# Optimization experiments

Measured on AMD Instinct MI355X. Metric: run time of the kernel, lower is better.

The kernel has to match this reference:

```python
import jax, jax.numpy as jnp
import numpy as np

N_NODES = 100000
N_EDGES = 1000000
F_IN = 8
HID = 64
VOCAB = 64
TXT_F = 64
SEQ = 10
N_CLASSES = 2


def setup_inputs() -> dict:
    key = jax.random.key(0)
    ks = jax.random.split(key, 16)
    inp = {
        "x": jax.random.normal(ks[0], (N_NODES, F_IN), dtype=jnp.float32),
        "edge_index": jax.random.randint(ks[1], (2, N_EDGES), 0, N_NODES, dtype=jnp.int32),
        "xtext": jax.random.randint(ks[2], (N_NODES, SEQ), 0, VOCAB, dtype=jnp.int32),
        # GCN layers (PyG convention: out = norm_agg(x @ W) + b)
        "conv1_w": jax.random.normal(ks[3], (F_IN, HID), dtype=jnp.float32) * 0.2,
        "conv1_b": jnp.zeros((HID,), jnp.float32),
        "conv2_w": jax.random.normal(ks[4], (HID, HID), dtype=jnp.float32) * 0.1,
        "conv2_b": jnp.zeros((HID,), jnp.float32),
        # embedding + GRU (torch layout: w_ih [3H, in], w_hh [3H, H])
        "embed": jax.random.normal(ks[5], (VOCAB, TXT_F), dtype=jnp.float32) * 0.1,
        "gru_w_ih": jax.random.normal(ks[6], (3 * HID, TXT_F), dtype=jnp.float32) * 0.1,
        "gru_w_hh": jax.random.normal(ks[7], (3 * HID, HID), dtype=jnp.float32) * 0.1,
        "gru_b_ih": jnp.zeros((3 * HID,), jnp.float32),
        "gru_b_hh": jnp.zeros((3 * HID,), jnp.float32),
        # pair MLPs (torch Linear layout: [out, in])
        "lin1_w": jax.random.normal(ks[8], (HID, 2 * HID), dtype=jnp.float32) * 0.1,
        "lin1_b": jnp.zeros((HID,), jnp.float32),
        "lin_text_w": jax.random.normal(ks[9], (HID, 2 * HID), dtype=jnp.float32) * 0.1,
        "lin_text_b": jnp.zeros((HID,), jnp.float32),
        "lin_final_w": jax.random.normal(ks[10], (N_CLASSES, 2 * HID), dtype=jnp.float32) * 0.1,
        "lin_final_b": jnp.zeros((N_CLASSES,), jnp.float32),
    }
    return inp


def _gcn_norm(edge_index, n_nodes):
    # PyG GCNConv default: add self loops, symmetric normalization
    loops = jnp.arange(n_nodes, dtype=edge_index.dtype)
    src = jnp.concatenate([edge_index[0], loops])
    dst = jnp.concatenate([edge_index[1], loops])
    deg = jax.ops.segment_sum(jnp.ones_like(dst, dtype=jnp.float32), dst, num_segments=n_nodes)
    dinv = jnp.where(deg > 0, jax.lax.rsqrt(deg), 0.0)
    norm = dinv[src] * dinv[dst]  # [E+N]
    return src, dst, norm


def _gcn(h, src, dst, norm, W, b, n_nodes):
    h = h @ W                              # [N, out]
    msg = h[src] * norm[:, None]           # gather + scale
    out = jax.ops.segment_sum(msg, dst, num_segments=n_nodes)
    return out + b


def _gru_last(xe, w_ih, w_hh, b_ih, b_hh):
    # xe: [N, T, F]; returns last hidden state [N, H]
    H = w_hh.shape[1]
    gi_all = jnp.einsum('ntf,gf->ntg', xe, w_ih) + b_ih  # precompute input gates [N,T,3H]
    gi_all = jnp.transpose(gi_all, (1, 0, 2))            # [T, N, 3H]

    def step(h, gi):
        gh = h @ w_hh.T + b_hh
        i_r, i_z, i_n = jnp.split(gi, 3, axis=-1)
        h_r, h_z, h_n = jnp.split(gh, 3, axis=-1)
        r = jax.nn.sigmoid(i_r + h_r)
        z = jax.nn.sigmoid(i_z + h_z)
        n = jnp.tanh(i_n + r * h_n)
        h = (1.0 - z) * n + z * h
        return h, None

    h0 = jnp.zeros((xe.shape[0], H), xe.dtype)
    h_last, _ = jax.lax.scan(step, h0, gi_all)
    return h_last


def reference(x, edge_index, xtext,
              conv1_w, conv1_b, conv2_w, conv2_b,
              embed, gru_w_ih, gru_w_hh, gru_b_ih, gru_b_hh,
              lin1_w, lin1_b, lin_text_w, lin_text_b, lin_final_w, lin_final_b):
    n = x.shape[0]
    src, dst, norm = _gcn_norm(edge_index, n)

    h = jax.nn.relu(_gcn(x, src, dst, norm, conv1_w, conv1_b, n))
    h = jax.nn.relu(_gcn(h, src, dst, norm, conv2_w, conv2_b, n))

    xe = embed[xtext]                                   # [N, T, F]
    textout = _gru_last(xe, gru_w_ih, gru_w_hh, gru_b_ih, gru_b_hh)  # [N, 64]

    s, t = edge_index[0], edge_index[1]
    xpair = jnp.concatenate([h[s], h[t]], axis=1)       # [E, 128]
    xpair = jax.nn.relu(xpair @ lin1_w.T + lin1_b)

    xpairtext = jnp.concatenate([textout[s], textout[t]], axis=1)
    xpairtext = jax.nn.relu(xpairtext @ lin_text_w.T + lin_text_b)

    xfin = jnp.concatenate([xpair, xpairtext], axis=1) @ lin_final_w.T + lin_final_b
    return jax.nn.log_softmax(xfin, axis=1)
```

## Files before the change

kernel.cpp:

```cpp
#include <hip/hip_runtime.h>
#include <stdint.h>

#define N_NODES 100000
#define N_EDGES 1000000
#define NBLK 391

typedef unsigned short u16;
typedef unsigned int u32;
typedef __attribute__((ext_vector_type(8))) short bshort8;
typedef __attribute__((ext_vector_type(4))) float f32x4;

__device__ __forceinline__ float bf2f(u16 u){ union{float f; u32 i;} x; x.i=((u32)u)<<16; return x.f; }
__device__ __forceinline__ u16 f2bf(float f){ union{float f; u32 i;} x; x.f=f; u32 r = x.i + 0x7FFFu + ((x.i>>16)&1u); return (u16)(r>>16); }

__device__ __forceinline__ float fexp2(float x){
#if __has_builtin(__builtin_amdgcn_exp2f)
    return __builtin_amdgcn_exp2f(x);
#else
    return exp2f(x);
#endif
}
__device__ __forceinline__ float frcp(float x){
#if __has_builtin(__builtin_amdgcn_rcpf)
    return __builtin_amdgcn_rcpf(x);
#else
    return 1.0f/x;
#endif
}
#define LOG2E 1.442695041f

__global__ void k_detect(const u16* __restrict__ x, int* flagp){
    __shared__ int cnt;
    if(threadIdx.x == 0) cnt = 0;
    __syncthreads();
    int c = 0;
    for(int i = threadIdx.x; i < 2048; i += 256){
        int e = (x[i] >> 7) & 0xFF;
        if(e >= 0x90) c++;
    }
    atomicAdd(&cnt, c);
    __syncthreads();
    if(threadIdx.x == 0) flagp[0] = (cnt > 64) ? 1 : 0;
}

#define CX    0
#define CW1   800000
#define CB1   800512
#define CW2   800576
#define CB2   804672
#define CEMB  804736
#define CWIH  808832
#define CWHH  821120
#define CBIH  833408
#define CBHH  833600
#define CL1W  833792
#define CL1B  841984
#define CLTW  842048
#define CLTB  850240
#define CLFW  850304
#define CLFB  850560
#define CTOT  850562

__device__ __forceinline__ float ldany(const void* p, int i, int fl){
    return fl ? ((const float*)p)[i] : bf2f(((const u16*)p)[i]);
}

#define NCONV 3323
#define B_W2  (NCONV)
#define B_WHH (B_W2 + 16)
#define B_L1A (B_WHH + 48)
#define B_L1B (B_L1A + 16)
#define B_LTA (B_L1B + 16)
#define B_LTB (B_LTA + 16)
#define B_GIT (B_LTB + 16)
#define B_TOT (B_GIT + 48)

__device__ __forceinline__ void packb_dev(const void* src, u16* dst,
                                          int K, int N, int ldk, int ldn,
                                          int fl, int i){
    if(i >= K*N) return;
    int k = i / N, n = i % N;
    int kt = k >> 5, kk = k & 31, q = kk >> 3, j = kk & 7;
    int nt = n >> 4, nn = n & 15;
    int KT = K >> 5;
    dst[(((nt*KT + kt)*64) + (q*16 + nn))*8 + j] = f2bf(ldany(src, k*ldk + n*ldn, fl));
}

__global__ void k_tables(const int* __restrict__ flagp,
                         const void* x, const void* w1, const void* b1, const void* w2,
                         const void* b2, const void* emb, const void* wih, const void* whh,
                         const void* bih, const void* bhh, const void* l1w, const void* l1b,
                         const void* ltw, const void* ltb, const void* lfw, const void* lfb,
                         float* __restrict__ canon,
                         u16* __restrict__ w2p, u16* __restrict__ whhp,
                         u16* __restrict__ l1pa, u16* __restrict__ l1pb,
                         u16* __restrict__ ltpa, u16* __restrict__ ltpb,
                         float* __restrict__ giT){
    int b = blockIdx.x, tid = threadIdx.x;
    int fl = *flagp;
    if(b < NCONV){
        int i = b*256 + tid;
        if(i >= CTOT) return;
        const void* p; int off;
        if     (i < CW1 ){ p = x;   off = i;        }
        else if(i < CB1 ){ p = w1;  off = i - CW1;  }
        else if(i < CW2 ){ p = b1;  off = i - CB1;  }
        else if(i < CB2 ){ p = w2;  off = i - CW2;  }
        else if(i < CEMB){ p = b2;  off = i - CB2;  }
        else if(i < CWIH){ p = emb; off = i - CEMB; }
        else if(i < CWHH){ p = wih; off = i - CWIH; }
        else if(i < CBIH){ p = whh; off = i - CWHH; }
        else if(i < CBHH){ p = bih; off = i - CBIH; }
        else if(i < CL1W){ p = bhh; off = i - CBHH; }
        else if(i < CL1B){ p = l1w; off = i - CL1W; }
        else if(i < CLTW){ p = l1b; off = i - CL1B; }
        else if(i < CLTB){ p = ltw; off = i - CLTW; }
        else if(i < CLFW){ p = ltb; off = i - CLTB; }
        else if(i < CLFB){ p = lfw; off = i - CLFW; }
        else             { p = lfb; off = i - CLFB; }
        float v = ldany(p, off, fl);
        canon[i] = (v == v && fabsf(v) < 1e30f) ? v : 0.f;
    }else if(b < B_WHH){
        packb_dev(w2, w2p, 64, 64, 64, 1, fl, (b - B_W2)*256 + tid);
    }else if(b < B_L1A){
        packb_dev(whh, whhp, 64, 192, 1, 64, fl, (b - B_WHH)*256 + tid);
    }else if(b < B_L1B){
        packb_dev(l1w, l1pa, 64, 64, 1, 128, fl, (b - B_L1A)*256 + tid);
    }else if(b < B_LTA){
        packb_dev((const void*)((const char*)l1w + (fl ? 64*4 : 64*2)),
                  l1pb, 64, 64, 1, 128, fl, (b - B_L1B)*256 + tid);
    }else if(b < B_LTB){
        packb_dev(ltw, ltpa, 64, 64, 1, 128, fl, (b - B_LTA)*256 + tid);
    }else if(b < B_GIT){
        packb_dev((const void*)((const char*)ltw + (fl ? 64*4 : 64*2)),
                  ltpb, 64, 64, 1, 128, fl, (b - B_LTB)*256 + tid);
    }else{
        int i = (b - B_GIT)*256 + tid;
        if(i >= 64*192) return;
        int v = i / 192, g = i % 192;
        float acc = ldany(bih, g, fl) + ((g < 128) ? ldany(bhh, g, fl) : 0.0f);
        for(int f = 0; f < 64; f++) acc += ldany(wih, g*64 + f, fl) * ldany(emb, v*64 + f, fl);
        int g3 = g >> 6, rem = g & 63, t = rem >> 4, col = rem & 15;
        giT[(((size_t)v*3 + g3)*16 + col)*4 + t] = acc;
    }
}

__global__ void k_hist(const int* __restrict__ ei, int* __restrict__ deg){
    int e = blockIdx.x*256 + threadIdx.x;
    if(e < N_EDGES) atomicAdd(&deg[ei[N_EDGES + e]], 1);
}
__global__ void k_scan1(const int* __restrict__ deg, int* __restrict__ rowptr,
                        int* __restrict__ bsum){
    __shared__ int sh[256];
    int tid = threadIdx.x;
    int i = blockIdx.x*256 + tid;
    int v = (i < N_NODES) ? deg[i] : 0;
    sh[tid] = v;
    __syncthreads();
    for(int off = 1; off < 256; off <<= 1){
        int t = (tid >= off) ? sh[tid - off] : 0;
        __syncthreads();
        sh[tid] += t;
        __syncthreads();
    }
    if(i < N_NODES) rowptr[i] = sh[tid] - v;
    if(tid == 255) bsum[blockIdx.x] = sh[255];
}
__global__ void k_scan2(int* __restrict__ bsum){
    __shared__ int sh[512];
    int tid = threadIdx.x;
    int v = (tid < NBLK) ? bsum[tid] : 0;
    sh[tid] = v;
    __syncthreads();
    for(int off = 1; off < 512; off <<= 1){
        int t = (tid >= off) ? sh[tid - off] : 0;
        __syncthreads();
        sh[tid] += t;
        __syncthreads();
    }
    if(tid < NBLK) bsum[tid] = sh[tid] - v;
}
__global__ void k_scan3(const int* __restrict__ deg, const int* __restrict__ bsum,
                        int* __restrict__ rowptr, int* __restrict__ cursor,
                        float* __restrict__ dinv){
    int i = blockIdx.x*256 + threadIdx.x;
    if(i < N_NODES){
        int r = rowptr[i] + bsum[i >> 8];
        rowptr[i] = r;
        cursor[i] = r;
        dinv[i] = rsqrtf((float)deg[i] + 1.0f);
    }
    if(i == 0) rowptr[N_NODES] = N_EDGES;
}
__global__ void k_fill(const int* __restrict__ ei, int* __restrict__ cursor,
                       int* __restrict__ el, int* __restrict__ dl, int* __restrict__ eid){
    int e = blockIdx.x*256 + threadIdx.x;
    if(e < N_EDGES){
        int s = ei[e], d = ei[N_EDGES + e];
        int pos = atomicAdd(&cursor[d], 1);
        el[pos] = s;
        dl[pos] = d;
        eid[pos] = e;
    }
}

__global__ void k_t1s(const float* __restrict__ cx, const float* __restrict__ cw1,
                      const float* __restrict__ dinv, u16* __restrict__ src){
    __shared__ float w[512];
    int t = threadIdx.x;
    w[t]       = cw1[t];
    w[t + 256] = cw1[t + 256];
    __syncthreads();
    int i = blockIdx.x*256 + t;
    int n = i >> 6, f = i & 63;
    const float* xr = cx + n*8;
    float acc = 0.f;
    #pragma unroll
    for(int k = 0; k < 8; k++) acc += xr[k] * w[k*64 + f];
    src[i] = f2bf(acc * dinv[n]);
}

__global__ __launch_bounds__(256)
void k_gather_ep(const int* __restrict__ rowptr, const int* __restrict__ el,
                 const u16* __restrict__ src, const float* __restrict__ dinv,
                 const float* __restrict__ b, u16* __restrict__ h, int ostride){
    int gid = blockIdx.x*256 + threadIdx.x;
    int node = gid >> 5, fp = (gid & 31)*2;
    int beg = rowptr[node], end = rowptr[node + 1];
    u32 self = *(const u32*)(src + (size_t)node*64 + fp);
    float acc0 = bf2f((u16)self), acc1 = bf2f((u16)(self >> 16));
    int i = beg;
    for(; i + 4 <= end; i += 4){
        int s0 = el[i], s1 = el[i+1], s2 = el[i+2], s3 = el[i+3];
        u32 a0 = *(const u32*)(src + (size_t)s0*64 + fp);
        u32 a1 = *(const u32*)(src + (size_t)s1*64 + fp);
        u32 a2 = *(const u32*)(src + (size_t)s2*64 + fp);
        u32 a3 = *(const u32*)(src + (size_t)s3*64 + fp);
        acc0 += bf2f((u16)a0); acc1 += bf2f((u16)(a0 >> 16));
        acc0 += bf2f((u16)a1); acc1 += bf2f((u16)(a1 >> 16));
        acc0 += bf2f((u16)a2); acc1 += bf2f((u16)(a2 >> 16));
        acc0 += bf2f((u16)a3); acc1 += bf2f((u16)(a3 >> 16));
    }
    for(; i < end; i++){
        u32 a = *(const u32*)(src + (size_t)el[i]*64 + fp);
        acc0 += bf2f((u16)a); acc1 += bf2f((u16)(a >> 16));
    }
    float dv = dinv[node];
    float r0 = fmaxf(dv*acc0 + b[fp],     0.f);
    float r1 = fmaxf(dv*acc1 + b[fp + 1], 0.f);
    *(u32*)(h + (size_t)node*ostride + fp) = (u32)f2bf(r0) | ((u32)f2bf(r1) << 16);
}

__global__ __launch_bounds__(256, 4)
void k_conv2(const u16* __restrict__ h, const u16* __restrict__ w2p,
             const float* __restrict__ dinv, u16* __restrict__ src){
    int wv = threadIdx.x >> 6, lane = threadIdx.x & 63;
    int g = blockIdx.x*4 + wv;
    if(g >= N_NODES/16) return;
    int q = lane >> 4, m = lane & 15, col = m;
    bshort8 a0 = *(const bshort8*)(h + (g*16 + m)*64 + q*8);
    bshort8 a1 = *(const bshort8*)(h + (g*16 + m)*64 + 32 + q*8);
    f32x4 acc[4];
    #pragma unroll
    for(int nt = 0; nt < 4; nt++){
        f32x4 c = {0.f,0.f,0.f,0.f};
        c = __builtin_amdgcn_mfma_f32_16x16x32_bf16(a0, *(const bshort8*)(w2p + ((nt*2+0)*64 + lane)*8), c, 0,0,0);
        c = __builtin_amdgcn_mfma_f32_16x16x32_bf16(a1, *(const bshort8*)(w2p + ((nt*2+1)*64 + lane)*8), c, 0,0,0);
        acc[nt] = c;
    }
    #pragma unroll
    for(int nt = 0; nt < 4; nt++)
        #pragma unroll
        for(int r = 0; r < 4; r++){
            int node = g*16 + q*4 + r;
            src[node*64 + nt*16 + col] = f2bf(acc[nt][r] * dinv[node]);
        }
}

__global__ __launch_bounds__(256, 4)
void k_gru(const int* __restrict__ xt, const u16* __restrict__ whhp,
           const float* __restrict__ giT, const float* __restrict__ bhh,
           u16* nodef, u32* __restrict__ udst,
           const u16* __restrict__ w1a, const u16* __restrict__ w1b,
           const u16* __restrict__ wta, const u16* __restrict__ wtb,
           const float* __restrict__ b1, const float* __restrict__ bt){
    __shared__ __align__(16) u16 wsh[12288];
    __shared__ __align__(16) u16 hsh[4][16][72];
    int tid = threadIdx.x;
    {
        const uint4* s = (const uint4*)whhp;
        uint4* d = (uint4*)wsh;
        #pragma unroll
        for(int i = 0; i < 6; i++) d[tid + 256*i] = s[tid + 256*i];
    }
    __syncthreads();

    int wv = tid >> 6, lane = tid & 63;
    int q = lane >> 4, m = lane & 15, col = m;
    int g = blockIdx.x*4 + wv;
    bool active = g < (N_NODES/16);
    int nb = active ? g*16 : 0;

    float bhhn[4];
    #pragma unroll
    for(int t = 0; t < 4; t++) bhhn[t] = bhh[128 + t*16 + col];

    const bshort8* wl = (const bshort8*)wsh;
    const u16* hp = &hsh[wv][m][0];

    float hc[4][4];
    #pragma unroll
    for(int t = 0; t < 4; t++)
        #pragma unroll
        for(int r = 0; r < 4; r++) hc[t][r] = 0.f;

    for(int s = 0; s < 10; s++){
        #pragma unroll
        for(int t = 0; t < 4; t++)
            #pragma unroll
            for(int r = 0; r < 4; r++)
                hsh[wv][q*4 + r][t*16 + col] = f2bf(hc[t][r]);

        asm volatile("" ::: "memory");
        bshort8 a0 = *(const bshort8*)(hp + q*8);
        bshort8 a1 = *(const bshort8*)(hp + 32 + q*8);

        int tok[4];
        #pragma unroll
        for(int r = 0; r < 4; r++) tok[r] = xt[(nb + q*4 + r)*10 + s] & 63;

        f32x4 acc[12];
        #pragma unroll
        for(int nt = 0; nt < 12; nt++){
            f32x4 c = {0.f,0.f,0.f,0.f};
            c = __builtin_amdgcn_mfma_f32_16x16x32_bf16(a0, wl[(nt*2+0)*64 + lane], c, 0,0,0);
            c = __builtin_amdgcn_mfma_f32_16x16x32_bf16(a1, wl[(nt*2+1)*64 + lane], c, 0,0,0);
            acc[nt] = c;
        }

        #pragma unroll
        for(int r = 0; r < 4; r++){
            const float4* gp = (const float4*)(giT + (size_t)tok[r]*192);
            float4 gr = gp[col];
            float4 gz = gp[16 + col];
            float4 gn = gp[32 + col];
            #pragma unroll
            for(int t = 0; t < 4; t++){
                float gir = ((const float*)&gr)[t];
                float giz = ((const float*)&gz)[t];
                float gin = ((const float*)&gn)[t];
                float rr = frcp(1.0f + fexp2(-LOG2E*(gir + acc[t][r])));
                float zz = frcp(1.0f + fexp2(-LOG2E*(giz + acc[4+t][r])));
                float narg = gin + rr*(acc[8+t][r] + bhhn[t]);
                float e2 = fexp2(2.0f*LOG2E*narg);
                float nn = 1.0f - 2.0f*frcp(e2 + 1.0f);
                hc[t][r] = nn + zz*(hc[t][r] - nn);
            }
        }
        asm volatile("" ::: "memory");
    }

    #pragma unroll
    for(int t = 0; t < 4; t++)
        #pragma unroll
        for(int r = 0; r < 4; r++)
            hsh[wv][q*4 + r][t*16 + col] = f2bf(hc[t][r]);
    asm volatile("" ::: "memory");
    bshort8 at0 = *(const bshort8*)(hp + q*8);
    bshort8 at1 = *(const bshort8*)(hp + 32 + q*8);
    const u16* row = nodef + (size_t)(nb + m)*128;
    bshort8 ah0 = *(const bshort8*)(row + q*8);
    bshort8 ah1 = *(const bshort8*)(row + 32 + q*8);

    u32* usrc = (u32*)nodef;
    #pragma unroll
    for(int nt = 0; nt < 4; nt++){
        f32x4 cu1 = {0.f,0.f,0.f,0.f}, cu2 = {0.f,0.f,0.f,0.f};
        f32x4 cv1 = {0.f,0.f,0.f,0.f}, cv2 = {0.f,0.f,0.f,0.f};
        cu1 = __builtin_amdgcn_mfma_f32_16x16x32_bf16(ah0, *(const bshort8*)(w1a + ((nt*2+0)*64 + lane)*8), cu1, 0,0,0);
        cu1 = __builtin_amdgcn_mfma_f32_16x16x32_bf16(ah1, *(const bshort8*)(w1a + ((nt*2+1)*64 + lane)*8), cu1, 0,0,0);
        cu2 = __builtin_amdgcn_mfma_f32_16x16x32_bf16(ah0, *(const bshort8*)(w1b + ((nt*2+0)*64 + lane)*8), cu2, 0,0,0);
        cu2 = __builtin_amdgcn_mfma_f32_16x16x32_bf16(ah1, *(const bshort8*)(w1b + ((nt*2+1)*64 + lane)*8), cu2, 0,0,0);
        cv1 = __builtin_amdgcn_mfma_f32_16x16x32_bf16(at0, *(const bshort8*)(wta + ((nt*2+0)*64 + lane)*8), cv1, 0,0,0);
        cv1 = __builtin_amdgcn_mfma_f32_16x16x32_bf16(at1, *(const bshort8*)(wta + ((nt*2+1)*64 + lane)*8), cv1, 0,0,0);
        cv2 = __builtin_amdgcn_mfma_f32_16x16x32_bf16(at0, *(const bshort8*)(wtb + ((nt*2+0)*64 + lane)*8), cv2, 0,0,0);
        cv2 = __builtin_amdgcn_mfma_f32_16x16x32_bf16(at1, *(const bshort8*)(wtb + ((nt*2+1)*64 + lane)*8), cv2, 0,0,0);
        if(active){
            int f = nt*16 + col;
            float b1f = b1[f], btf = bt[f];
            #pragma unroll
            for(int r = 0; r < 4; r++){
                int node = nb + q*4 + r;
                u32 pa = (u32)f2bf(cu1[r] + b1f) | ((u32)f2bf(cv1[r] + btf) << 16);
                u32 pb = (u32)f2bf(cu2[r]) | ((u32)f2bf(cv2[r]) << 16);
                usrc[(size_t)node*64 + f] = pa;
                udst[(size_t)node*64 + f] = pb;
            }
        }
    }
}

__global__ __launch_bounds__(256, 6)
void k_edge2(const int* __restrict__ el, const int* __restrict__ dl, const int* __restrict__ eid,
             const u32* __restrict__ usrc, const u32* __restrict__ udst,
             const float* __restrict__ wfin, const float* __restrict__ bfin,
             const int* __restrict__ flagp, void* __restrict__ out){
    int tid = threadIdx.x;
    int lane = tid & 63;
    int q = lane >> 4, f0 = lane & 15;
    int wid = (blockIdx.x*256 + tid) >> 6;
    int nwv = (gridDim.x*256) >> 6;
    int fl = *flagp;

    float wp0[4], wp1[4], wt0[4], wt1[4];
    #pragma unroll
    for(int t = 0; t < 4; t++){
        int f = 4*f0 + t;
        wp0[t] = wfin[f];        wt0[t] = wfin[64 + f];
        wp1[t] = wfin[128 + f];  wt1[t] = wfin[192 + f];
    }
    float bf0 = bfin[0], bf1 = bfin[1];

    for(int grp = wid; grp < N_EDGES/4; grp += nwv){
        int e = grp*4 + q;
        int s = el[e], d = dl[e];
        uint4 us4 = *((const uint4*)(usrc + (size_t)s*64) + f0);
        uint4 ud4 = *((const uint4*)(udst + (size_t)d*64) + f0);
        u32 us[4] = {us4.x, us4.y, us4.z, us4.w};
        u32 ud[4] = {ud4.x, ud4.y, ud4.z, ud4.w};
        float s0 = 0.f, s1 = 0.f;
        #pragma unroll
        for(int t = 0; t < 4; t++){
            float u1 = __uint_as_float(us[t] << 16);
            float v1 = __uint_as_float(us[t] & 0xffff0000u);
            float u2 = __uint_as_float(ud[t] << 16);
            float v2 = __uint_as_float(ud[t] & 0xffff0000u);
            float xp = fmaxf(u1 + u2, 0.f);
            float xq = fmaxf(v1 + v2, 0.f);
            s0 += xp*wp0[t] + xq*wt0[t];
            s1 += xp*wp1[t] + xq*wt1[t];
        }
        #pragma unroll
        for(int msk = 1; msk < 16; msk <<= 1){
            s0 += __shfl_xor(s0, msk, 64);
            s1 += __shfl_xor(s1, msk, 64);
        }
        if(f0 == 0){
            float a = s0 + bf0, b = s1 + bf1;
            float mx = fmaxf(a, b);
            float lse = mx + __logf(__expf(a - mx) + __expf(b - mx));
            int oi = eid[e];
            if(fl){
                float2 v; v.x = a - lse; v.y = b - lse;
                ((float2*)out)[oi] = v;
            }else{
                u32 pack = (u32)f2bf(a - lse) | ((u32)f2bf(b - lse) << 16);
                ((u32*)out)[oi] = pack;
            }
        }
    }
}

static const size_t O_FLAG   = 0;
static const size_t O_CANON  = 4096;
static const size_t O_GIT    = 3407872;
static const size_t O_W2P    = 3457024;
static const size_t O_WHHP   = 3465216;
static const size_t O_L1PA   = 3489792;
static const size_t O_L1PB   = 3497984;
static const size_t O_LTPA   = 3506176;
static const size_t O_LTPB   = 3514368;
static const size_t O_DINV   = 3522560;
static const size_t O_DEG    = 3922560;
static const size_t O_ROWPTR = 4322560;
static const size_t O_CURSOR = 4722688;
static const size_t O_BSUM   = 5122688;
static const size_t O_EL     = 5124736;
static const size_t O_DL     = 9125888;
static const size_t O_EID    = 13125888;
static const size_t O_SRC    = 17125888;
static const size_t O_H1     = 29925888;
static const size_t O_UDST   = 17125888;
static const size_t O_NODEF  = 42725888;

extern "C" void kernel_launch(void* const* d_in, const int* in_sizes, int n_in,
                              void* d_out, int out_size, void* d_ws, size_t ws_size,
                              hipStream_t stream){
    const void* x    = d_in[0];
    const int*  ei   = (const int*)d_in[1];
    const int*  xt   = (const int*)d_in[2];

    char* ws = (char*)d_ws;
    int*   flagp  = (int*)(ws + O_FLAG);
    float* canon  = (float*)(ws + O_CANON);
    float* giT    = (float*)(ws + O_GIT);
    u16*   w2p    = (u16*)(ws + O_W2P);
    u16*   whhp   = (u16*)(ws + O_WHHP);
    u16*   l1pa   = (u16*)(ws + O_L1PA);
    u16*   l1pb   = (u16*)(ws + O_L1PB);
    u16*   ltpa   = (u16*)(ws + O_LTPA);
    u16*   ltpb   = (u16*)(ws + O_LTPB);
    float* dinv   = (float*)(ws + O_DINV);
    int*   deg    = (int*)(ws + O_DEG);
    int*   rowptr = (int*)(ws + O_ROWPTR);
    int*   cursor = (int*)(ws + O_CURSOR);
    int*   bsum   = (int*)(ws + O_BSUM);
    int*   el     = (int*)(ws + O_EL);
    int*   dl     = (int*)(ws + O_DL);
    int*   eid    = (int*)(ws + O_EID);
    u16*   src    = (u16*)(ws + O_SRC);
    u16*   hbuf1  = (u16*)(ws + O_H1);
    u32*   udst   = (u32*)(ws + O_UDST);
    u16*   nodef  = (u16*)(ws + O_NODEF);

    k_detect<<<1, 256, 0, stream>>>((const u16*)x, flagp);
    k_tables<<<B_TOT, 256, 0, stream>>>(flagp,
        x, d_in[3], d_in[4], d_in[5], d_in[6], d_in[7], d_in[8], d_in[9],
        d_in[10], d_in[11], d_in[12], d_in[13], d_in[14], d_in[15], d_in[16], d_in[17],
        canon, w2p, whhp, l1pa, l1pb, ltpa, ltpb, giT);

    const float* cx   = canon + CX;
    const float* cw1  = canon + CW1;
    const float* cb1  = canon + CB1;
    const float* cb2  = canon + CB2;
    const float* cbhh = canon + CBHH;
    const float* cl1b = canon + CL1B;
    const float* cltb = canon + CLTB;
    const float* clfw = canon + CLFW;
    const float* clfb = canon + CLFB;

    hipMemsetAsync(deg, 0, (size_t)N_NODES*4, stream);
    k_hist <<<(N_EDGES+255)/256, 256, 0, stream>>>(ei, deg);
    k_scan1<<<NBLK, 256, 0, stream>>>(deg, rowptr, bsum);
    k_scan2<<<1, 512, 0, stream>>>(bsum);
    k_scan3<<<NBLK, 256, 0, stream>>>(deg, bsum, rowptr, cursor, dinv);
    k_fill <<<(N_EDGES+255)/256, 256, 0, stream>>>(ei, cursor, el, dl, eid);

    k_t1s<<<N_NODES*64/256, 256, 0, stream>>>(cx, cw1, dinv, src);
    k_gather_ep<<<N_NODES*32/256, 256, 0, stream>>>(rowptr, el, src, dinv, cb1, hbuf1, 64);

    k_conv2<<<(N_NODES/16 + 3)/4, 256, 0, stream>>>(hbuf1, w2p, dinv, src);
    k_gather_ep<<<N_NODES*32/256, 256, 0, stream>>>(rowptr, el, src, dinv, cb2, nodef, 128);

    k_gru<<<(N_NODES/16 + 3)/4, 256, 0, stream>>>(xt, whhp, giT, cbhh,
                                                  nodef, udst, l1pa, l1pb, ltpa, ltpb,
                                                  cl1b, cltb);

    k_edge2<<<4096, 256, 0, stream>>>(el, dl, eid, (const u32*)nodef, udst,
                                      clfw, clfb, flagp, d_out);
}
```

Baseline: 450.4 us.

## Aggregate 8-wide inputs before conv1 matmul instead of gathering 64-wide features

Reorders the first GCN layer so neighbour aggregation runs on the 8-feature scaled input (fp32), followed by the 8x64 weight multiply, bias and ReLU. Since aggregation is linear this is algebraically equivalent, and the per-edge gather traffic drops from 64 bf16 values to 8 fp32 values. The degree-scaled input is produced inside the scan kernel. It adds a small agg8 buffer and changes rounding, since the accumulation is now fp32 before the matmul instead of over bf16 projected features.

```diff
diff --git a/kernel.cpp b/kernel.cpp
--- a/kernel.cpp
+++ b/kernel.cpp
@@ -182,13 +182,19 @@
 }
 __global__ void k_scan3(const int* __restrict__ deg, const int* __restrict__ bsum,
                         int* __restrict__ rowptr, int* __restrict__ cursor,
-                        float* __restrict__ dinv){
+                        float* __restrict__ dinv, const float* __restrict__ cx,
+                        float* __restrict__ xs){
     int i = blockIdx.x*256 + threadIdx.x;
     if(i < N_NODES){
         int r = rowptr[i] + bsum[i >> 8];
         rowptr[i] = r;
         cursor[i] = r;
-        dinv[i] = rsqrtf((float)deg[i] + 1.0f);
+        float dv = rsqrtf((float)deg[i] + 1.0f);
+        dinv[i] = dv;
+        const float* xr = cx + (size_t)i*8;
+        float* xo = xs + (size_t)i*8;
+        #pragma unroll
+        for(int k = 0; k < 8; k++) xo[k] = xr[k]*dv;
     }
     if(i == 0) rowptr[N_NODES] = N_EDGES;
 }
@@ -204,8 +210,38 @@
     }
 }
 
-__global__ void k_t1s(const float* __restrict__ cx, const float* __restrict__ cw1,
-                      const float* __restrict__ dinv, u16* __restrict__ src){
+__global__ __launch_bounds__(256)
+void k_gather8(const int* __restrict__ rowptr, const int* __restrict__ el,
+               const float* __restrict__ xs, float* __restrict__ agg8){
+    int gid = blockIdx.x*256 + threadIdx.x;
+    int node = gid >> 2, fp = (gid & 3)*2;
+    if(node >= N_NODES) return;
+    int beg = rowptr[node], end = rowptr[node + 1];
+    float2 self = *(const float2*)(xs + (size_t)node*8 + fp);
+    float a0 = self.x, a1 = self.y;
+    int i = beg;
+    for(; i + 4 <= end; i += 4){
+        int s0 = el[i], s1 = el[i+1], s2 = el[i+2], s3 = el[i+3];
+        float2 v0 = *(const float2*)(xs + (size_t)s0*8 + fp);
+        float2 v1 = *(const float2*)(xs + (size_t)s1*8 + fp);
+        float2 v2 = *(const float2*)(xs + (size_t)s2*8 + fp);
+        float2 v3 = *(const float2*)(xs + (size_t)s3*8 + fp);
+        a0 += v0.x; a1 += v0.y;
+        a0 += v1.x; a1 += v1.y;
+        a0 += v2.x; a1 += v2.y;
+        a0 += v3.x; a1 += v3.y;
+    }
+    for(; i < end; i++){
+        float2 v = *(const float2*)(xs + (size_t)el[i]*8 + fp);
+        a0 += v.x; a1 += v.y;
+    }
+    float2 o; o.x = a0; o.y = a1;
+    *(float2*)(agg8 + (size_t)node*8 + fp) = o;
+}
+
+__global__ void k_conv1(const float* __restrict__ agg8, const float* __restrict__ cw1,
+                        const float* __restrict__ dinv, const float* __restrict__ b1,
+                        u16* __restrict__ h1){
     __shared__ float w[512];
     int t = threadIdx.x;
     w[t]       = cw1[t];
@@ -213,11 +249,11 @@
     __syncthreads();
     int i = blockIdx.x*256 + t;
     int n = i >> 6, f = i & 63;
-    const float* xr = cx + n*8;
+    const float* ar = agg8 + (size_t)n*8;
     float acc = 0.f;
     #pragma unroll
-    for(int k = 0; k < 8; k++) acc += xr[k] * w[k*64 + f];
-    src[i] = f2bf(acc * dinv[n]);
+    for(int k = 0; k < 8; k++) acc += ar[k] * w[k*64 + f];
+    h1[(size_t)n*64 + f] = f2bf(fmaxf(dinv[n]*acc + b1[f], 0.f));
 }
 
 __global__ __launch_bounds__(256)
@@ -479,6 +515,8 @@
 static const size_t O_DL     = 9125888;
 static const size_t O_EID    = 13125888;
 static const size_t O_SRC    = 17125888;
+static const size_t O_XS     = 17125888;
+static const size_t O_AGG8   = 20325888;
 static const size_t O_H1     = 29925888;
 static const size_t O_UDST   = 17125888;
 static const size_t O_NODEF  = 42725888;
@@ -509,6 +547,8 @@
     int*   dl     = (int*)(ws + O_DL);
     int*   eid    = (int*)(ws + O_EID);
     u16*   src    = (u16*)(ws + O_SRC);
+    float* xs     = (float*)(ws + O_XS);
+    float* agg8   = (float*)(ws + O_AGG8);
     u16*   hbuf1  = (u16*)(ws + O_H1);
     u32*   udst   = (u32*)(ws + O_UDST);
     u16*   nodef  = (u16*)(ws + O_NODEF);
@@ -533,11 +573,11 @@
     k_hist <<<(N_EDGES+255)/256, 256, 0, stream>>>(ei, deg);
     k_scan1<<<NBLK, 256, 0, stream>>>(deg, rowptr, bsum);
     k_scan2<<<1, 512, 0, stream>>>(bsum);
-    k_scan3<<<NBLK, 256, 0, stream>>>(deg, bsum, rowptr, cursor, dinv);
+    k_scan3<<<NBLK, 256, 0, stream>>>(deg, bsum, rowptr, cursor, dinv, cx, xs);
     k_fill <<<(N_EDGES+255)/256, 256, 0, stream>>>(ei, cursor, el, dl, eid);
 
-    k_t1s<<<N_NODES*64/256, 256, 0, stream>>>(cx, cw1, dinv, src);
-    k_gather_ep<<<N_NODES*32/256, 256, 0, stream>>>(rowptr, el, src, dinv, cb1, hbuf1, 64);
+    k_gather8<<<(N_NODES*4 + 255)/256, 256, 0, stream>>>(rowptr, el, xs, agg8);
+    k_conv1<<<N_NODES*64/256, 256, 0, stream>>>(agg8, cw1, dinv, cb1, hbuf1);
 
     k_conv2<<<(N_NODES/16 + 3)/4, 256, 0, stream>>>(hbuf1, w2p, dinv, src);
     k_gather_ep<<<N_NODES*32/256, 256, 0, stream>>>(rowptr, el, src, dinv, cb2, nodef, 128);
```

Measured after the change: 428.7 us. -4.8%, faster.
